# Kernel optimization log

Hardware: AMD Instinct MI355X
Metric: run time of the kernel (lower is better)

The kernel has to match this reference:

```python
import jax, jax.numpy as jnp
import numpy as np

B, N, DIM = 4, 2048, 512
H, DH = 8, 64  # heads, dim_head; inner_dim = H*DH = 512
SCALE = DH ** -0.5
EPS = 1e-5


def _layer_norm(x, gamma):
    # LayerNorm with learned gamma and beta fixed to zeros (beta is a buffer)
    mu = jnp.mean(x, axis=-1, keepdims=True)
    var = jnp.var(x, axis=-1, keepdims=True)
    return (x - mu) * jax.lax.rsqrt(var + EPS) * gamma


def setup_inputs() -> dict:
    key = jax.random.key(0)
    ks = jax.random.split(key, 6)
    x = jax.random.normal(ks[0], (B, N, DIM), jnp.float32)
    mask = jax.random.bernoulli(ks[1], 0.9, (B, N))  # bool [b, n]
    gamma = jnp.ones((DIM,), jnp.float32)            # pre-attn LayerNorm gamma
    Wq = jax.random.normal(ks[2], (DIM, H * DH), jnp.float32) * 0.02
    Wkv = jax.random.normal(ks[3], (DIM, 2 * DH), jnp.float32) * 0.02  # shared single KV head (MQA)
    null_kv = jax.random.normal(ks[4], (2, DH), jnp.float32)
    Wout = jax.random.normal(ks[5], (H * DH, DIM), jnp.float32) * 0.02
    out_gamma = jnp.ones((DIM,), jnp.float32)        # post-proj LayerNorm gamma
    return {"x": x, "mask": mask, "gamma": gamma, "Wq": Wq, "Wkv": Wkv,
            "null_kv": null_kv, "Wout": Wout, "out_gamma": out_gamma}


def reference(x, mask, gamma, Wq, Wkv, null_kv, Wout, out_gamma):
    b, n, _ = x.shape
    xn = _layer_norm(x, gamma)
    # queries: per-head; keys/values: single shared head (multi-query)
    q = (xn @ Wq).reshape(b, n, H, DH).transpose(0, 2, 1, 3) * SCALE  # [b,h,n,d]
    kv = xn @ Wkv                                                     # [b,n,2d]
    k, v = kv[..., :DH], kv[..., DH:]                                 # [b,n,d]
    # prepend learned null key/value (attention sink) shared across batch
    nk = jnp.broadcast_to(null_kv[0], (b, 1, DH))
    nv = jnp.broadcast_to(null_kv[1], (b, 1, DH))
    k = jnp.concatenate([nk, k], axis=1)  # [b, n+1, d]
    v = jnp.concatenate([nv, v], axis=1)
    sim = jnp.einsum('bhid,bjd->bhij', q, k)  # [b,h,n,n+1]
    # mask padded with True for the null token, broadcast over heads/queries
    m = jnp.concatenate([jnp.ones((b, 1), bool), mask], axis=1)
    max_neg = -jnp.finfo(sim.dtype).max
    sim = jnp.where(m[:, None, None, :], sim, max_neg)
    attn = jax.nn.softmax(sim.astype(jnp.float32), axis=-1).astype(x.dtype)
    out = jnp.einsum('bhij,bjd->bhid', attn, v)       # [b,h,n,d]
    out = out.transpose(0, 2, 1, 3).reshape(b, n, H * DH)
    return _layer_norm(out @ Wout, out_gamma)
```

## Files before the change

### kernel.cpp

```cpp
#include <hip/hip_runtime.h>

typedef __attribute__((ext_vector_type(8)))  short bf16x8;
typedef __attribute__((ext_vector_type(4)))  float f32x4;
typedef __attribute__((ext_vector_type(16))) float f32x16;
typedef __attribute__((ext_vector_type(4)))  unsigned u32x4;

#define Nx 2048
#define CTXx 2049
#define KCAP 2112
#define QSCALE 0.125f

__device__ __forceinline__ short f2bs(float x){
    unsigned u = __builtin_bit_cast(unsigned, x);
    u = (u + 0x7fffu + ((u >> 16) & 1u)) >> 16;
    return (short)u;
}
__device__ __forceinline__ unsigned pack2(float lo, float hi){
    return ((unsigned)(unsigned short)f2bs(hi) << 16) | (unsigned)(unsigned short)f2bs(lo);
}

__global__ void __launch_bounds__(256) ln1_kernel(const float* __restrict__ x,
                                                  const float* __restrict__ g,
                                                  short* __restrict__ out){
    int w = threadIdx.x >> 6, lane = threadIdx.x & 63;
    size_t row = (size_t)blockIdx.x * 4 + w;
    const float* xr = x + row * 512 + lane * 8;
    float4 a = *(const float4*)xr;
    float4 b = *(const float4*)(xr + 4);
    float s = a.x + a.y + a.z + a.w + b.x + b.y + b.z + b.w;
    float q = a.x*a.x + a.y*a.y + a.z*a.z + a.w*a.w
            + b.x*b.x + b.y*b.y + b.z*b.z + b.w*b.w;
    #pragma unroll
    for (int m = 1; m < 64; m <<= 1){ s += __shfl_xor(s, m, 64); q += __shfl_xor(q, m, 64); }
    float mu  = s * (1.f / 512.f);
    float var = fmaxf(q * (1.f / 512.f) - mu * mu, 0.f);
    float r   = rsqrtf(var + 1e-5f);
    const float* gr = g + lane * 8;
    float4 g0 = *(const float4*)gr;
    float4 g1 = *(const float4*)(gr + 4);
    bf16x8 o;
    o[0] = f2bs((a.x - mu) * r * g0.x); o[1] = f2bs((a.y - mu) * r * g0.y);
    o[2] = f2bs((a.z - mu) * r * g0.z); o[3] = f2bs((a.w - mu) * r * g0.w);
    o[4] = f2bs((b.x - mu) * r * g1.x); o[5] = f2bs((b.y - mu) * r * g1.y);
    o[6] = f2bs((b.z - mu) * r * g1.z); o[7] = f2bs((b.w - mu) * r * g1.w);
    *(bf16x8*)(out + row * 512 + lane * 8) = o;
}

__global__ void __launch_bounds__(256) ln2_kernel(const float* __restrict__ z,
                                                  const float* __restrict__ g,
                                                  float* __restrict__ out){
    int w = threadIdx.x >> 6, lane = threadIdx.x & 63;
    size_t row = (size_t)blockIdx.x * 4 + w;
    const float* xr = z + row * 512 + lane * 8;
    float4 a = *(const float4*)xr;
    float4 b = *(const float4*)(xr + 4);
    float s = a.x + a.y + a.z + a.w + b.x + b.y + b.z + b.w;
    float q = a.x*a.x + a.y*a.y + a.z*a.z + a.w*a.w
            + b.x*b.x + b.y*b.y + b.z*b.z + b.w*b.w;
    #pragma unroll
    for (int m = 1; m < 64; m <<= 1){ s += __shfl_xor(s, m, 64); q += __shfl_xor(q, m, 64); }
    float mu  = s * (1.f / 512.f);
    float var = fmaxf(q * (1.f / 512.f) - mu * mu, 0.f);
    float r   = rsqrtf(var + 1e-5f);
    const float* gr = g + lane * 8;
    float4 g0 = *(const float4*)gr;
    float4 g1 = *(const float4*)(gr + 4);
    float4 o0, o1;
    o0.x = (a.x - mu) * r * g0.x; o0.y = (a.y - mu) * r * g0.y;
    o0.z = (a.z - mu) * r * g0.z; o0.w = (a.w - mu) * r * g0.w;
    o1.x = (b.x - mu) * r * g1.x; o1.y = (b.y - mu) * r * g1.y;
    o1.z = (b.z - mu) * r * g1.z; o1.w = (b.w - mu) * r * g1.w;
    float* op = out + row * 512 + lane * 8;
    *(float4*)op = o0; *(float4*)(op + 4) = o1;
}

__global__ void __launch_bounds__(256) prep_kernel(const float* __restrict__ Wq,
                                                   const float* __restrict__ Wkv,
                                                   const float* __restrict__ Wout,
                                                   const float* __restrict__ nkv,
                                                   short* __restrict__ WcatT,
                                                   short* __restrict__ WoutT,
                                                   short* __restrict__ kb,
                                                   short* __restrict__ vbt){
    int t = threadIdx.x;
    if (blockIdx.x == 2304){
        int b = t >> 6, d = t & 63;
        kb[((size_t)b * KCAP) * 64 + d] = f2bs(nkv[d]);
        vbt[((size_t)b * 64 + d) * KCAP + 0] = f2bs(nkv[64 + d]);
        return;
    }
    int idx = blockIdx.x * 256 + t;
    if (idx < 327680){
        int n = idx >> 9, k = idx & 511;
        float v = (n < 512) ? Wq[(size_t)k * 512 + n] : Wkv[(size_t)k * 128 + (n - 512)];
        WcatT[idx] = f2bs(v);
    } else {
        int j = idx - 327680;
        int n = j >> 9, k = j & 511;
        WoutT[j] = f2bs(Wout[(size_t)k * 512 + n]);
    }
}

template<int MODE>
__global__ void __launch_bounds__(256, 2) gemm_mfma(const short* __restrict__ A,
                                                    const short* __restrict__ BwT,
                                                    short* __restrict__ qb,
                                                    short* __restrict__ kb,
                                                    short* __restrict__ vbt,
                                                    float* __restrict__ C){
    __shared__ short As[128][72];
    __shared__ short Bs[128][72];
    int t = threadIdx.x;
    int lane = t & 63, w = t >> 6;
    int l16 = lane & 15, quad = lane >> 4;
    int wm = w & 1, wn = w >> 1;
    int row0 = blockIdx.y * 128, col0 = blockIdx.x * 128;
    f32x4 acc[4][4];
    #pragma unroll
    for (int i = 0; i < 4; i++)
        #pragma unroll
        for (int j = 0; j < 4; j++) acc[i][j] = (f32x4){0.f, 0.f, 0.f, 0.f};
    int ar = t >> 1, ak = (t & 1) * 32;
    for (int k0 = 0; k0 < 512; k0 += 64){
        __syncthreads();
        {
            const short* ap = A + (size_t)(row0 + ar) * 512 + k0 + ak;
            int4 a0 = *(const int4*)(ap);
            int4 a1 = *(const int4*)(ap + 8);
            int4 a2 = *(const int4*)(ap + 16);
            int4 a3 = *(const int4*)(ap + 24);
            *(int4*)&As[ar][ak]      = a0;
            *(int4*)&As[ar][ak + 8]  = a1;
            *(int4*)&As[ar][ak + 16] = a2;
            *(int4*)&As[ar][ak + 24] = a3;
        }
        {
            const short* bp = BwT + (size_t)(col0 + ar) * 512 + k0 + ak;
            int4 b0 = *(const int4*)(bp);
            int4 b1 = *(const int4*)(bp + 8);
            int4 b2 = *(const int4*)(bp + 16);
            int4 b3 = *(const int4*)(bp + 24);
            *(int4*)&Bs[ar][ak]      = b0;
            *(int4*)&Bs[ar][ak + 8]  = b1;
            *(int4*)&Bs[ar][ak + 16] = b2;
            *(int4*)&Bs[ar][ak + 24] = b3;
        }
        __syncthreads();
        #pragma unroll
        for (int ks = 0; ks < 2; ks++){
            bf16x8 af[4], bfr[4];
            #pragma unroll
            for (int mt = 0; mt < 4; mt++)
                af[mt] = *(const bf16x8*)&As[wm * 64 + mt * 16 + l16][ks * 32 + quad * 8];
            #pragma unroll
            for (int nt = 0; nt < 4; nt++)
                bfr[nt] = *(const bf16x8*)&Bs[wn * 64 + nt * 16 + l16][ks * 32 + quad * 8];
            #pragma unroll
            for (int mt = 0; mt < 4; mt++)
                #pragma unroll
                for (int nt = 0; nt < 4; nt++)
                    acc[mt][nt] = __builtin_amdgcn_mfma_f32_16x16x32_bf16(af[mt], bfr[nt], acc[mt][nt], 0, 0, 0);
        }
    }
    #pragma unroll
    for (int mt = 0; mt < 4; mt++)
        #pragma unroll
        for (int nt = 0; nt < 4; nt++)
            #pragma unroll
            for (int r = 0; r < 4; r++){
                int row = row0 + wm * 64 + mt * 16 + quad * 4 + r;
                int col = col0 + wn * 64 + nt * 16 + l16;
                float v = acc[mt][nt][r];
                if (MODE == 0){
                    int bb = row >> 11, ii = row & 2047;
                    if (col < 512){
                        qb[(size_t)row * 512 + col] = f2bs(v * QSCALE);
                    } else if (col < 576){
                        kb[((size_t)bb * KCAP + ii + 1) * 64 + (col - 512)] = f2bs(v);
                    } else {
                        vbt[((size_t)bb * 64 + (col - 576)) * KCAP + ii + 1] = f2bs(v);
                    }
                } else {
                    C[(size_t)row * 512 + col] = v;
                }
            }
}

__global__ void __launch_bounds__(256, 2) attn_kernel(const short* __restrict__ qb,
                                                      const short* __restrict__ kb,
                                                      const short* __restrict__ vbt,
                                                      const int* __restrict__ mask,
                                                      short* __restrict__ ob){
    __shared__ short Ks[64][72];
    __shared__ short Vt[64][72];
    __shared__ float Ls[4][32];
    int t = threadIdx.x;
    int lane = t & 63, w = t >> 6;
    int n32 = lane & 31, hb = lane >> 5;
    int b = blockIdx.y, i0 = blockIdx.x * 16;
    int head = 2 * w + (n32 >> 4), row = i0 + (n32 & 15);
    bf16x8 qf[4];
    {
        const short* qp = qb + ((size_t)(b * Nx + row)) * 512 + head * 64 + hb * 8;
        #pragma unroll
        for (int ks = 0; ks < 4; ks++) qf[ks] = *(const bf16x8*)(qp + ks * 16);
    }
    f32x16 oacc[2];
    #pragma unroll
    for (int i = 0; i < 2; i++)
        #pragma unroll
        for (int j = 0; j < 16; j++) oacc[i][j] = 0.f;
    float lsum = 0.f;

    int skey = t >> 2, sd = (t & 3) * 16;
    int vd   = t >> 2, vk = (t & 3) * 16;
    const short* kgp = kb  + (size_t)b * KCAP * 64 + skey * 64 + sd;
    const short* vgp = vbt + ((size_t)b * 64 + vd) * KCAP + vk;
    const int* mrow = mask + b * Nx;

    int4 pk0, pk1, pv0, pv1;
    int mok;
    {
        pk0 = *(const int4*)(kgp);
        pk1 = *(const int4*)(kgp + 8);
        pv0 = *(const int4*)(vgp);
        pv1 = *(const int4*)(vgp + 8);
        int jg = lane;
        mok = (jg == 0) ? 1 : ((jg < CTXx) ? mrow[jg - 1] : 0);
    }
    for (int j0 = 0; j0 < KCAP; j0 += 64){
        __syncthreads();
        *(int4*)&Ks[skey][sd]     = pk0;
        *(int4*)&Ks[skey][sd + 8] = pk1;
        *(int4*)&Vt[vd][vk]       = pv0;
        *(int4*)&Vt[vd][vk + 8]   = pv1;
        unsigned long long bal = __ballot(mok != 0);
        __syncthreads();
        int jn = j0 + 64;
        if (jn < KCAP){
            pk0 = *(const int4*)(kgp + (size_t)jn * 64);
            pk1 = *(const int4*)(kgp + (size_t)jn * 64 + 8);
            pv0 = *(const int4*)(vgp + jn);
            pv1 = *(const int4*)(vgp + jn + 8);
            int jg = jn + lane;
            mok = (jg < CTXx) ? mrow[jg - 1] : 0;
        }
        f32x16 sf[2];
        #pragma unroll
        for (int i = 0; i < 2; i++)
            #pragma unroll
            for (int j = 0; j < 16; j++) sf[i][j] = 0.f;
        #pragma unroll
        for (int ks = 0; ks < 4; ks++){
            #pragma unroll
            for (int kt = 0; kt < 2; kt++){
                bf16x8 kf = *(const bf16x8*)&Ks[kt * 32 + n32][ks * 16 + hb * 8];
                sf[kt] = __builtin_amdgcn_mfma_f32_32x32x16_bf16(kf, qf[ks], sf[kt], 0, 0, 0);
            }
        }
        unsigned mlo = (unsigned)(bal >> (4 * hb));
        unsigned mhi = (unsigned)(bal >> (32 + 4 * hb));
        unsigned pg[8][2];
        #pragma unroll
        for (int kt = 0; kt < 2; kt++){
            unsigned mm = kt ? mhi : mlo;
            #pragma unroll
            for (int g4 = 0; g4 < 4; g4++){
                float p[4];
                #pragma unroll
                for (int tt = 0; tt < 4; tt++){
                    float e = __expf(sf[kt][g4 * 4 + tt]);
                    p[tt] = ((mm >> (8 * g4 + tt)) & 1u) ? e : 0.f;
                    lsum += p[tt];
                }
                pg[kt * 4 + g4][0] = pack2(p[0], p[1]);
                pg[kt * 4 + g4][1] = pack2(p[2], p[3]);
            }
        }
        #pragma unroll
        for (int s = 0; s < 4; s++){
            unsigned slo = hb ? pg[2 * s][0] : pg[2 * s + 1][0];
            unsigned shi = hb ? pg[2 * s][1] : pg[2 * s + 1][1];
            unsigned rlo = (unsigned)__shfl_xor((int)slo, 32, 64);
            unsigned rhi = (unsigned)__shfl_xor((int)shi, 32, 64);
            unsigned q0 = hb ? rlo : pg[2 * s][0];
            unsigned q1 = hb ? rhi : pg[2 * s][1];
            unsigned q2 = hb ? pg[2 * s + 1][0] : rlo;
            unsigned q3 = hb ? pg[2 * s + 1][1] : rhi;
            bf16x8 pa = __builtin_bit_cast(bf16x8, (u32x4){q0, q1, q2, q3});
            #pragma unroll
            for (int nt = 0; nt < 2; nt++){
                bf16x8 vf = *(const bf16x8*)&Vt[nt * 32 + n32][s * 16 + hb * 8];
                oacc[nt] = __builtin_amdgcn_mfma_f32_32x32x16_bf16(pa, vf, oacc[nt], 0, 0, 0);
            }
        }
    }
    float L = lsum + __shfl_xor(lsum, 32, 64);
    if (hb == 0) Ls[w][n32] = 1.f / L;
    __syncthreads();
    #pragma unroll
    for (int nt = 0; nt < 2; nt++)
        #pragma unroll
        for (int r = 0; r < 16; r++){
            int hr = (r & 3) + 8 * (r >> 2) + 4 * hb;
            float o = oacc[nt][r] * Ls[w][hr];
            int grow = i0 + (hr & 15);
            int ghead = 2 * w + (hr >> 4);
            ob[((size_t)(b * Nx + grow)) * 512 + ghead * 64 + nt * 32 + n32] = f2bs(o);
        }
}

extern "C" void kernel_launch(void* const* d_in, const int* in_sizes, int n_in,
                              void* d_out, int out_size, void* d_ws, size_t ws_size,
                              hipStream_t stream){
    const float* x     = (const float*)d_in[0];
    const int*   mask  = (const int*)  d_in[1];
    const float* gamma = (const float*)d_in[2];
    const float* Wq    = (const float*)d_in[3];
    const float* Wkv   = (const float*)d_in[4];
    const float* nkv   = (const float*)d_in[5];
    const float* Wout  = (const float*)d_in[6];
    const float* og    = (const float*)d_in[7];
    float* out = (float*)d_out;

    short* xnb   = (short*)d_ws;
    short* qb    = xnb + (size_t)4194304;
    short* kb    = qb  + (size_t)4194304;
    short* vbt   = kb  + (size_t)540672;
    short* ob    = vbt + (size_t)540672;
    short* WcatT = ob  + (size_t)4194304;
    short* WoutT = WcatT + (size_t)327680;
    float* zb    = (float*)d_ws;

    ln1_kernel  <<<2048, 256, 0, stream>>>(x, gamma, xnb);
    prep_kernel <<<2305, 256, 0, stream>>>(Wq, Wkv, Wout, nkv, WcatT, WoutT, kb, vbt);
    gemm_mfma<0><<<dim3(5, 64), 256, 0, stream>>>(xnb, WcatT, qb, kb, vbt, nullptr);
    attn_kernel <<<dim3(128, 4), 256, 0, stream>>>(qb, kb, vbt, mask, ob);
    gemm_mfma<1><<<dim3(4, 64), 256, 0, stream>>>(ob, WoutT, nullptr, nullptr, nullptr, zb);
    ln2_kernel  <<<2048, 256, 0, stream>>>(zb, og, out);
}
```

Measured before the change: 200.8 us.

## Use exp2 softmax, truncating bf16 pack, register-local P fragments, tiled weight transpose

Result: faster. 186.1 us (-7.3%).

```diff
diff --git a/kernel.cpp b/kernel.cpp
--- a/kernel.cpp
+++ b/kernel.cpp
@@ -8,15 +8,16 @@
 #define Nx 2048
 #define CTXx 2049
 #define KCAP 2112
-#define QSCALE 0.125f
+#define QSCALE 0.18033688f
 
 __device__ __forceinline__ short f2bs(float x){
     unsigned u = __builtin_bit_cast(unsigned, x);
     u = (u + 0x7fffu + ((u >> 16) & 1u)) >> 16;
     return (short)u;
 }
-__device__ __forceinline__ unsigned pack2(float lo, float hi){
-    return ((unsigned)(unsigned short)f2bs(hi) << 16) | (unsigned)(unsigned short)f2bs(lo);
+__device__ __forceinline__ unsigned pack_trunc(float a, float b){
+    return __builtin_amdgcn_perm(__builtin_bit_cast(unsigned, b),
+                                 __builtin_bit_cast(unsigned, a), 0x07060302u);
 }
 
 __global__ void __launch_bounds__(256) ln1_kernel(const float* __restrict__ x,
@@ -82,23 +83,36 @@
                                                    short* __restrict__ WoutT,
                                                    short* __restrict__ kb,
                                                    short* __restrict__ vbt){
-    int t = threadIdx.x;
-    if (blockIdx.x == 2304){
+    int bid = blockIdx.x, t = threadIdx.x;
+    if (bid == 144){
         int b = t >> 6, d = t & 63;
         kb[((size_t)b * KCAP) * 64 + d] = f2bs(nkv[d]);
         vbt[((size_t)b * 64 + d) * KCAP + 0] = f2bs(nkv[64 + d]);
         return;
     }
-    int idx = blockIdx.x * 256 + t;
-    if (idx < 327680){
-        int n = idx >> 9, k = idx & 511;
-        float v = (n < 512) ? Wq[(size_t)k * 512 + n] : Wkv[(size_t)k * 128 + (n - 512)];
-        WcatT[idx] = f2bs(v);
-    } else {
-        int j = idx - 327680;
-        int n = j >> 9, k = j & 511;
-        WoutT[j] = f2bs(Wout[(size_t)k * 512 + n]);
-    }
+    __shared__ float ls[64][65];
+    bool isOut = (bid >= 80);
+    int b2 = isOut ? bid - 80 : bid;
+    int ntile = isOut ? (b2 & 7) : (b2 % 10);
+    int ktile = isOut ? (b2 >> 3) : (b2 / 10);
+    int n0 = ntile * 64, k0 = ktile * 64;
+    #pragma unroll
+    for (int rr = 0; rr < 64; rr += 16){
+        int r = rr + (t >> 4), c = (t & 15) * 4;
+        float4 v;
+        if (isOut)            v = *(const float4*)(Wout + (size_t)(k0 + r) * 512 + n0 + c);
+        else if (n0 < 512)    v = *(const float4*)(Wq   + (size_t)(k0 + r) * 512 + n0 + c);
+        else                  v = *(const float4*)(Wkv  + (size_t)(k0 + r) * 128 + (n0 - 512) + c);
+        ls[c + 0][r] = v.x; ls[c + 1][r] = v.y; ls[c + 2][r] = v.z; ls[c + 3][r] = v.w;
+    }
+    __syncthreads();
+    int rn = t >> 2, kc = (t & 3) * 16;
+    short tmp[16];
+    #pragma unroll
+    for (int j = 0; j < 16; j++) tmp[j] = f2bs(ls[rn][kc + j]);
+    short* dst = (isOut ? WoutT : WcatT) + (size_t)(n0 + rn) * 512 + k0 + kc;
+    *(int4*)dst       = *(int4*)&tmp[0];
+    *(int4*)(dst + 8) = *(int4*)&tmp[8];
 }
 
 template<int MODE>
@@ -232,8 +246,8 @@
         __syncthreads();
         *(int4*)&Ks[skey][sd]     = pk0;
         *(int4*)&Ks[skey][sd + 8] = pk1;
-        *(int4*)&Vt[vd][vk]       = pv0;
-        *(int4*)&Vt[vd][vk + 8]   = pv1;
+        *(int4*)&Vt[vd][vk]       = make_int4(pv0.x, pv0.y, pv1.x, pv1.y);
+        *(int4*)&Vt[vd][vk + 8]   = make_int4(pv0.z, pv0.w, pv1.z, pv1.w);
         unsigned long long bal = __ballot(mok != 0);
         __syncthreads();
         int jn = j0 + 64;
@@ -269,25 +283,18 @@
                 float p[4];
                 #pragma unroll
                 for (int tt = 0; tt < 4; tt++){
-                    float e = __expf(sf[kt][g4 * 4 + tt]);
+                    float e = __builtin_amdgcn_exp2f(sf[kt][g4 * 4 + tt]);
                     p[tt] = ((mm >> (8 * g4 + tt)) & 1u) ? e : 0.f;
                     lsum += p[tt];
                 }
-                pg[kt * 4 + g4][0] = pack2(p[0], p[1]);
-                pg[kt * 4 + g4][1] = pack2(p[2], p[3]);
+                pg[kt * 4 + g4][0] = pack_trunc(p[0], p[1]);
+                pg[kt * 4 + g4][1] = pack_trunc(p[2], p[3]);
             }
         }
         #pragma unroll
         for (int s = 0; s < 4; s++){
-            unsigned slo = hb ? pg[2 * s][0] : pg[2 * s + 1][0];
-            unsigned shi = hb ? pg[2 * s][1] : pg[2 * s + 1][1];
-            unsigned rlo = (unsigned)__shfl_xor((int)slo, 32, 64);
-            unsigned rhi = (unsigned)__shfl_xor((int)shi, 32, 64);
-            unsigned q0 = hb ? rlo : pg[2 * s][0];
-            unsigned q1 = hb ? rhi : pg[2 * s][1];
-            unsigned q2 = hb ? pg[2 * s + 1][0] : rlo;
-            unsigned q3 = hb ? pg[2 * s + 1][1] : rhi;
-            bf16x8 pa = __builtin_bit_cast(bf16x8, (u32x4){q0, q1, q2, q3});
+            bf16x8 pa = __builtin_bit_cast(bf16x8,
+                (u32x4){pg[2 * s][0], pg[2 * s][1], pg[2 * s + 1][0], pg[2 * s + 1][1]});
             #pragma unroll
             for (int nt = 0; nt < 2; nt++){
                 bf16x8 vf = *(const bf16x8*)&Vt[nt * 32 + n32][s * 16 + hb * 8];
@@ -333,7 +340,7 @@
     float* zb    = (float*)d_ws;
 
     ln1_kernel  <<<2048, 256, 0, stream>>>(x, gamma, xnb);
-    prep_kernel <<<2305, 256, 0, stream>>>(Wq, Wkv, Wout, nkv, WcatT, WoutT, kb, vbt);
+    prep_kernel <<<145, 256, 0, stream>>>(Wq, Wkv, Wout, nkv, WcatT, WoutT, kb, vbt);
     gemm_mfma<0><<<dim3(5, 64), 256, 0, stream>>>(xnb, WcatT, qb, kb, vbt, nullptr);
     attn_kernel <<<dim3(128, 4), 256, 0, stream>>>(qb, kb, vbt, mask, ob);
     gemm_mfma<1><<<dim3(4, 64), 256, 0, stream>>>(ob, WoutT, nullptr, nullptr, nullptr, zb);
```
